# Kernel tuning notes

Hardware: AMD Instinct MI355X
Metric: run time of the kernel (lower is better)

## Reference

```python
import jax, jax.numpy as jnp
import numpy as np

N_NODES = 100000
N_ANCHORS = 32
EMB_DIM = 64


def setup_inputs() -> dict:
    key = jax.random.key(0)
    k1, k2, k3, k4, k5 = jax.random.split(key, 5)
    embeds = jax.random.normal(k1, (N_NODES, EMB_DIM), dtype=jnp.float32)
    dists_array = jax.random.uniform(k2, (N_NODES, N_ANCHORS), dtype=jnp.float32)
    # torch Linear(2*D, D): y = x @ W.T + b; we store W already transposed [2D, D]
    W_hidden = jax.random.normal(k3, (2 * EMB_DIM, EMB_DIM), dtype=jnp.float32) * (1.0 / np.sqrt(2 * EMB_DIM))
    b_hidden = jax.random.normal(k4, (EMB_DIM,), dtype=jnp.float32) * 0.01
    anchorset_id = jax.random.randint(k5, (N_ANCHORS,), 0, N_NODES)
    return {
        "embeds": embeds,
        "dists_array": dists_array,
        "W_hidden": W_hidden,
        "b_hidden": b_hidden,
        "anchorset_id": anchorset_id,
    }


def reference(embeds, dists_array, W_hidden, b_hidden, anchorset_id):
    # embeds: [N, D]; dists_array: [N, A]; anchorset_id: [A]
    set_emb = embeds[anchorset_id]                         # gather -> [A, D]
    msg_anchor = dists_array[:, :, None] * set_emb[None]   # [N, A, D]
    self_feat = jnp.broadcast_to(embeds[:, None, :], msg_anchor.shape)  # [N, A, D]
    messages = jnp.concatenate((msg_anchor, self_feat), axis=-1)        # [N, A, 2D]
    hidden = jnp.einsum('nae,ed->nad', messages, W_hidden) + b_hidden   # [N, A, D]
    return hidden.mean(axis=1)                              # [N, D]
```

## Files before the change

kernel.cpp:

```cpp
#include <hip/hip_runtime.h>
#include <cstdint>
#include <cstddef>


#define N_NODES 100000
#define DIM     64
#define NB      256
#define S       256

__device__ __forceinline__ void fma4(float4& a, float x, const float4& w) {
    a.x += x * w.x; a.y += x * w.y; a.z += x * w.z; a.w += x * w.w;
}

__global__ __launch_bounds__(256) void pnn_prep(
    const float* __restrict__ embeds,
    const float* __restrict__ W,
    const int*   __restrict__ aid,
    float*       __restrict__ P)
{
    const int t = blockIdx.x * 256 + threadIdx.x;
    const int a = t >> 6, d = t & 63;
    const float* se = embeds + (size_t)aid[a] * DIM;
    float s = 0.f;
    #pragma unroll
    for (int e = 0; e < DIM; ++e) s += se[e] * W[e * DIM + d];
    P[t] = s * (1.0f / 32.0f);
}

__global__ __launch_bounds__(256, 2) void pnn_main(
    const float* __restrict__ embeds,
    const float* __restrict__ dists,
    const float* __restrict__ P,
    const float* __restrict__ W,
    const float* __restrict__ bias,
    float* __restrict__ out)
{
    __shared__ float sw[4096];
    __shared__ float sn[32 * S];

    const int tid = threadIdx.x;
    const int n0  = blockIdx.x * NB;
    const int n   = n0 + tid;
    const bool valid = (n < N_NODES);
    const int d0  = (tid & 7) * 8;
    const int nl0 = (tid >> 3) * 8;

    float4 dv[8];
    {
        const float4* dg = (const float4*)(dists + (size_t)n * 32);
        #pragma unroll
        for (int g = 0; g < 8; ++g) dv[g] = valid ? dg[g] : make_float4(0.f, 0.f, 0.f, 0.f);
    }
    {
        const float4* Pg = (const float4*)P;
        float4 p0 = Pg[tid], p1 = Pg[tid + 256];
        ((float4*)sw)[tid] = p0; ((float4*)sw)[tid + 256] = p1;
    }
    float4 acc[8][2];
    {
        float4 b0 = *(const float4*)(bias + d0);
        float4 b1 = *(const float4*)(bias + d0 + 4);
        #pragma unroll
        for (int j = 0; j < 8; ++j) { acc[j][0] = b0; acc[j][1] = b1; }
    }
    #pragma unroll
    for (int g = 0; g < 8; ++g) {
        float* p = &sn[(4 * g) * S + tid];
        p[0] = dv[g].x; p[S] = dv[g].y; p[2 * S] = dv[g].z; p[3 * S] = dv[g].w;
    }
    __syncthreads();

    float4 ev[8];
    {
        const float4* eg = (const float4*)(embeds + (size_t)n * DIM);
        #pragma unroll
        for (int g = 0; g < 8; ++g) ev[g] = valid ? eg[g] : make_float4(0.f, 0.f, 0.f, 0.f);
    }

    #pragma unroll 4
    for (int a = 0; a < 32; ++a) {
        float4 x0 = *(const float4*)&sn[a * S + nl0];
        float4 x1 = *(const float4*)&sn[a * S + nl0 + 4];
        float4 w0 = *(const float4*)&sw[a * DIM + d0];
        float4 w1 = *(const float4*)&sw[a * DIM + d0 + 4];
        fma4(acc[0][0], x0.x, w0); fma4(acc[0][1], x0.x, w1);
        fma4(acc[1][0], x0.y, w0); fma4(acc[1][1], x0.y, w1);
        fma4(acc[2][0], x0.z, w0); fma4(acc[2][1], x0.z, w1);
        fma4(acc[3][0], x0.w, w0); fma4(acc[3][1], x0.w, w1);
        fma4(acc[4][0], x1.x, w0); fma4(acc[4][1], x1.x, w1);
        fma4(acc[5][0], x1.y, w0); fma4(acc[5][1], x1.y, w1);
        fma4(acc[6][0], x1.z, w0); fma4(acc[6][1], x1.z, w1);
        fma4(acc[7][0], x1.w, w0); fma4(acc[7][1], x1.w, w1);
    }
    __syncthreads();

    {
        const float4* Wg = (const float4*)(W + 64 * DIM);
        float4 a0 = Wg[tid], a1 = Wg[tid + 256];
        ((float4*)sw)[tid] = a0; ((float4*)sw)[tid + 256] = a1;
    }
    #pragma unroll
    for (int g = 0; g < 8; ++g) {
        float* p = &sn[(4 * g) * S + tid];
        p[0] = ev[g].x; p[S] = ev[g].y; p[2 * S] = ev[g].z; p[3 * S] = ev[g].w;
    }
    __syncthreads();

    {
        const float4* eg = (const float4*)(embeds + (size_t)n * DIM);
        #pragma unroll
        for (int g = 0; g < 8; ++g) ev[g] = valid ? eg[8 + g] : make_float4(0.f, 0.f, 0.f, 0.f);
    }

    #pragma unroll 4
    for (int e = 0; e < 32; ++e) {
        float4 x0 = *(const float4*)&sn[e * S + nl0];
        float4 x1 = *(const float4*)&sn[e * S + nl0 + 4];
        float4 w0 = *(const float4*)&sw[e * DIM + d0];
        float4 w1 = *(const float4*)&sw[e * DIM + d0 + 4];
        fma4(acc[0][0], x0.x, w0); fma4(acc[0][1], x0.x, w1);
        fma4(acc[1][0], x0.y, w0); fma4(acc[1][1], x0.y, w1);
        fma4(acc[2][0], x0.z, w0); fma4(acc[2][1], x0.z, w1);
        fma4(acc[3][0], x0.w, w0); fma4(acc[3][1], x0.w, w1);
        fma4(acc[4][0], x1.x, w0); fma4(acc[4][1], x1.x, w1);
        fma4(acc[5][0], x1.y, w0); fma4(acc[5][1], x1.y, w1);
        fma4(acc[6][0], x1.z, w0); fma4(acc[6][1], x1.z, w1);
        fma4(acc[7][0], x1.w, w0); fma4(acc[7][1], x1.w, w1);
    }
    __syncthreads();

    {
        const float4* Wg = (const float4*)(W + 64 * DIM + 2048);
        float4 a0 = Wg[tid], a1 = Wg[tid + 256];
        ((float4*)sw)[tid] = a0; ((float4*)sw)[tid + 256] = a1;
    }
    #pragma unroll
    for (int g = 0; g < 8; ++g) {
        float* p = &sn[(4 * g) * S + tid];
        p[0] = ev[g].x; p[S] = ev[g].y; p[2 * S] = ev[g].z; p[3 * S] = ev[g].w;
    }
    __syncthreads();

    #pragma unroll 4
    for (int e = 0; e < 32; ++e) {
        float4 x0 = *(const float4*)&sn[e * S + nl0];
        float4 x1 = *(const float4*)&sn[e * S + nl0 + 4];
        float4 w0 = *(const float4*)&sw[e * DIM + d0];
        float4 w1 = *(const float4*)&sw[e * DIM + d0 + 4];
        fma4(acc[0][0], x0.x, w0); fma4(acc[0][1], x0.x, w1);
        fma4(acc[1][0], x0.y, w0); fma4(acc[1][1], x0.y, w1);
        fma4(acc[2][0], x0.z, w0); fma4(acc[2][1], x0.z, w1);
        fma4(acc[3][0], x0.w, w0); fma4(acc[3][1], x0.w, w1);
        fma4(acc[4][0], x1.x, w0); fma4(acc[4][1], x1.x, w1);
        fma4(acc[5][0], x1.y, w0); fma4(acc[5][1], x1.y, w1);
        fma4(acc[6][0], x1.z, w0); fma4(acc[6][1], x1.z, w1);
        fma4(acc[7][0], x1.w, w0); fma4(acc[7][1], x1.w, w1);
    }

    #pragma unroll
    for (int j = 0; j < 8; ++j) {
        const int nn = n0 + nl0 + j;
        if (nn < N_NODES) {
            float* po = out + (size_t)nn * DIM + d0;
            *(float4*)po       = acc[j][0];
            *(float4*)(po + 4) = acc[j][1];
        }
    }
}

extern "C" void kernel_launch(void* const* d_in, const int* in_sizes, int n_in,
                              void* d_out, int out_size, void* d_ws, size_t ws_size,
                              hipStream_t stream) {
    const float* embeds = (const float*)d_in[0];
    const float* dists  = (const float*)d_in[1];
    const float* W      = (const float*)d_in[2];
    const float* bias   = (const float*)d_in[3];
    const int*   aid    = (const int*)d_in[4];
    float* out = (float*)d_out;

    float* P = (float*)d_ws;

    pnn_prep<<<8, 256, 0, stream>>>(embeds, W, aid, P);
    const int grid = (N_NODES + NB - 1) / NB;
    pnn_main<<<grid, 256, 0, stream>>>(embeds, dists, P, W, bias, out);
}
```

Measured before the change: 110.3 us.

## Replace LDS-tiled GEMM with one-node-per-thread register accumulation and uniform weight reads

Drops the shared-memory transpose and tiling. Each thread now owns one node and keeps all 64 output accumulators in registers. Weights (P and the second half of W) are read directly from global memory with wave-uniform addresses, which should become scalar loads or broadcasts. Blocks shrink to 64 threads, and the next chunk of each node's row is prefetched while the current one is processed. This removes LDS traffic and barriers, but each thread reads its own 384-byte row with strided per-lane accesses, which coalesces poorly, and register pressure rises, which may lower occupancy.

```diff
diff --git a/kernel.cpp b/kernel.cpp
--- a/kernel.cpp
+++ b/kernel.cpp
@@ -5,12 +5,6 @@
 
 #define N_NODES 100000
 #define DIM     64
-#define NB      256
-#define S       256
-
-__device__ __forceinline__ void fma4(float4& a, float x, const float4& w) {
-    a.x += x * w.x; a.y += x * w.y; a.z += x * w.z; a.w += x * w.w;
-}
 
 __global__ __launch_bounds__(256) void pnn_prep(
     const float* __restrict__ embeds,
@@ -27,7 +21,7 @@
     P[t] = s * (1.0f / 32.0f);
 }
 
-__global__ __launch_bounds__(256, 2) void pnn_main(
+__global__ __launch_bounds__(64) void pnn_main(
     const float* __restrict__ embeds,
     const float* __restrict__ dists,
     const float* __restrict__ P,
@@ -35,136 +29,56 @@
     const float* __restrict__ bias,
     float* __restrict__ out)
 {
-    __shared__ float sw[4096];
-    __shared__ float sn[32 * S];
+    const int n = blockIdx.x * 64 + threadIdx.x;
+    const bool valid = (n < N_NODES);
+    const size_t nc = valid ? (size_t)n : (size_t)(N_NODES - 1);
 
-    const int tid = threadIdx.x;
-    const int n0  = blockIdx.x * NB;
-    const int n   = n0 + tid;
-    const bool valid = (n < N_NODES);
-    const int d0  = (tid & 7) * 8;
-    const int nl0 = (tid >> 3) * 8;
+    float acc[DIM];
+    #pragma unroll
+    for (int d = 0; d < DIM; ++d) acc[d] = bias[d];
 
-    float4 dv[8];
-    {
-        const float4* dg = (const float4*)(dists + (size_t)n * 32);
+    const float4* drow = (const float4*)(dists  + nc * 32);
+    const float4* erow = (const float4*)(embeds + nc * (size_t)DIM);
+    const float*  W2   = W + 64 * DIM;
+
+    float4 x0 = drow[0], x1 = drow[1];
+    float4 p0 = erow[0], p1 = erow[1];
+
+    #pragma unroll 1
+    for (int eb = 0; eb < 4; ++eb) {
+        float4 nx0 = drow[(2 * eb + 2) & 7];
+        float4 nx1 = drow[(2 * eb + 3) & 7];
+        const float xs[8] = {x0.x, x0.y, x0.z, x0.w, x1.x, x1.y, x1.z, x1.w};
+        const float* wr = P + eb * 8 * DIM;
         #pragma unroll
-        for (int g = 0; g < 8; ++g) dv[g] = valid ? dg[g] : make_float4(0.f, 0.f, 0.f, 0.f);
-    }
-    {
-        const float4* Pg = (const float4*)P;
-        float4 p0 = Pg[tid], p1 = Pg[tid + 256];
-        ((float4*)sw)[tid] = p0; ((float4*)sw)[tid + 256] = p1;
-    }
-    float4 acc[8][2];
-    {
-        float4 b0 = *(const float4*)(bias + d0);
-        float4 b1 = *(const float4*)(bias + d0 + 4);
-        #pragma unroll
-        for (int j = 0; j < 8; ++j) { acc[j][0] = b0; acc[j][1] = b1; }
-    }
-    #pragma unroll
-    for (int g = 0; g < 8; ++g) {
-        float* p = &sn[(4 * g) * S + tid];
-        p[0] = dv[g].x; p[S] = dv[g].y; p[2 * S] = dv[g].z; p[3 * S] = dv[g].w;
-    }
-    __syncthreads();
-
-    float4 ev[8];
-    {
-        const float4* eg = (const float4*)(embeds + (size_t)n * DIM);
-        #pragma unroll
-        for (int g = 0; g < 8; ++g) ev[g] = valid ? eg[g] : make_float4(0.f, 0.f, 0.f, 0.f);
+        for (int j = 0; j < 8; ++j) {
+            #pragma unroll
+            for (int d = 0; d < DIM; ++d)
+                acc[d] += xs[j] * wr[j * DIM + d];
+        }
+        x0 = nx0; x1 = nx1;
     }
 
-    #pragma unroll 4
-    for (int a = 0; a < 32; ++a) {
-        float4 x0 = *(const float4*)&sn[a * S + nl0];
-        float4 x1 = *(const float4*)&sn[a * S + nl0 + 4];
-        float4 w0 = *(const float4*)&sw[a * DIM + d0];
-        float4 w1 = *(const float4*)&sw[a * DIM + d0 + 4];
-        fma4(acc[0][0], x0.x, w0); fma4(acc[0][1], x0.x, w1);
-        fma4(acc[1][0], x0.y, w0); fma4(acc[1][1], x0.y, w1);
-        fma4(acc[2][0], x0.z, w0); fma4(acc[2][1], x0.z, w1);
-        fma4(acc[3][0], x0.w, w0); fma4(acc[3][1], x0.w, w1);
-        fma4(acc[4][0], x1.x, w0); fma4(acc[4][1], x1.x, w1);
-        fma4(acc[5][0], x1.y, w0); fma4(acc[5][1], x1.y, w1);
-        fma4(acc[6][0], x1.z, w0); fma4(acc[6][1], x1.z, w1);
-        fma4(acc[7][0], x1.w, w0); fma4(acc[7][1], x1.w, w1);
-    }
-    __syncthreads();
-
-    {
-        const float4* Wg = (const float4*)(W + 64 * DIM);
-        float4 a0 = Wg[tid], a1 = Wg[tid + 256];
-        ((float4*)sw)[tid] = a0; ((float4*)sw)[tid + 256] = a1;
-    }
-    #pragma unroll
-    for (int g = 0; g < 8; ++g) {
-        float* p = &sn[(4 * g) * S + tid];
-        p[0] = ev[g].x; p[S] = ev[g].y; p[2 * S] = ev[g].z; p[3 * S] = ev[g].w;
-    }
-    __syncthreads();
-
-    {
-        const float4* eg = (const float4*)(embeds + (size_t)n * DIM);
+    #pragma unroll 1
+    for (int eb = 0; eb < 8; ++eb) {
+        float4 nx0 = erow[(2 * eb + 2) & 15];
+        float4 nx1 = erow[(2 * eb + 3) & 15];
+        const float xs[8] = {p0.x, p0.y, p0.z, p0.w, p1.x, p1.y, p1.z, p1.w};
+        const float* wr = W2 + eb * 8 * DIM;
         #pragma unroll
-        for (int g = 0; g < 8; ++g) ev[g] = valid ? eg[8 + g] : make_float4(0.f, 0.f, 0.f, 0.f);
+        for (int j = 0; j < 8; ++j) {
+            #pragma unroll
+            for (int d = 0; d < DIM; ++d)
+                acc[d] += xs[j] * wr[j * DIM + d];
+        }
+        p0 = nx0; p1 = nx1;
     }
 
-    #pragma unroll 4
-    for (int e = 0; e < 32; ++e) {
-        float4 x0 = *(const float4*)&sn[e * S + nl0];
-        float4 x1 = *(const float4*)&sn[e * S + nl0 + 4];
-        float4 w0 = *(const float4*)&sw[e * DIM + d0];
-        float4 w1 = *(const float4*)&sw[e * DIM + d0 + 4];
-        fma4(acc[0][0], x0.x, w0); fma4(acc[0][1], x0.x, w1);
-        fma4(acc[1][0], x0.y, w0); fma4(acc[1][1], x0.y, w1);
-        fma4(acc[2][0], x0.z, w0); fma4(acc[2][1], x0.z, w1);
-        fma4(acc[3][0], x0.w, w0); fma4(acc[3][1], x0.w, w1);
-        fma4(acc[4][0], x1.x, w0); fma4(acc[4][1], x1.x, w1);
-        fma4(acc[5][0], x1.y, w0); fma4(acc[5][1], x1.y, w1);
-        fma4(acc[6][0], x1.z, w0); fma4(acc[6][1], x1.z, w1);
-        fma4(acc[7][0], x1.w, w0); fma4(acc[7][1], x1.w, w1);
-    }
-    __syncthreads();
-
-    {
-        const float4* Wg = (const float4*)(W + 64 * DIM + 2048);
-        float4 a0 = Wg[tid], a1 = Wg[tid + 256];
-        ((float4*)sw)[tid] = a0; ((float4*)sw)[tid + 256] = a1;
-    }
-    #pragma unroll
-    for (int g = 0; g < 8; ++g) {
-        float* p = &sn[(4 * g) * S + tid];
-        p[0] = ev[g].x; p[S] = ev[g].y; p[2 * S] = ev[g].z; p[3 * S] = ev[g].w;
-    }
-    __syncthreads();
-
-    #pragma unroll 4
-    for (int e = 0; e < 32; ++e) {
-        float4 x0 = *(const float4*)&sn[e * S + nl0];
-        float4 x1 = *(const float4*)&sn[e * S + nl0 + 4];
-        float4 w0 = *(const float4*)&sw[e * DIM + d0];
-        float4 w1 = *(const float4*)&sw[e * DIM + d0 + 4];
-        fma4(acc[0][0], x0.x, w0); fma4(acc[0][1], x0.x, w1);
-        fma4(acc[1][0], x0.y, w0); fma4(acc[1][1], x0.y, w1);
-        fma4(acc[2][0], x0.z, w0); fma4(acc[2][1], x0.z, w1);
-        fma4(acc[3][0], x0.w, w0); fma4(acc[3][1], x0.w, w1);
-        fma4(acc[4][0], x1.x, w0); fma4(acc[4][1], x1.x, w1);
-        fma4(acc[5][0], x1.y, w0); fma4(acc[5][1], x1.y, w1);
-        fma4(acc[6][0], x1.z, w0); fma4(acc[6][1], x1.z, w1);
-        fma4(acc[7][0], x1.w, w0); fma4(acc[7][1], x1.w, w1);
-    }
-
-    #pragma unroll
-    for (int j = 0; j < 8; ++j) {
-        const int nn = n0 + nl0 + j;
-        if (nn < N_NODES) {
-            float* po = out + (size_t)nn * DIM + d0;
-            *(float4*)po       = acc[j][0];
-            *(float4*)(po + 4) = acc[j][1];
-        }
+    if (valid) {
+        float4* po = (float4*)(out + (size_t)n * DIM);
+        #pragma unroll
+        for (int g = 0; g < 16; ++g)
+            po[g] = make_float4(acc[4 * g], acc[4 * g + 1], acc[4 * g + 2], acc[4 * g + 3]);
     }
 }
 
@@ -181,6 +95,6 @@
     float* P = (float*)d_ws;
 
     pnn_prep<<<8, 256, 0, stream>>>(embeds, W, aid, P);
-    const int grid = (N_NODES + NB - 1) / NB;
-    pnn_main<<<grid, 256, 0, stream>>>(embeds, dists, P, W, bias, out);
+    const int grid = (N_NODES + 63) / 64;
+    pnn_main<<<grid, 64, 0, stream>>>(embeds, dists, P, W, bias, out);
 }
```

New measurement: 122.3 us. 1.11x slower.
